# Optimization experiments

Measured on AMD Instinct MI355X. Metric: run time of the kernel, lower is better.

The kernel has to match this reference:

```python
import jax, jax.numpy as jnp
import numpy as np

# ---- module config (init kwargs) ----
EMB = 256
HIDDEN = 256
L, H, P = 4, 8, 4
CH = HIDDEN // H
PADDING_MODE = "zeros"   # 'zeros' or 'border'
ALIGN_CORNERS = False
# feature pyramid level shapes (height, width), static
SHAPES = np.array([[128, 128], [64, 64], [32, 32], [16, 16]], dtype=np.int32)
LEVEL_STARTS = np.concatenate([[0], np.cumsum(SHAPES.prod(-1))[:-1]]).astype(np.int32)

B, N = 8, 1024
I = int(SHAPES.prod(-1).sum())  # 21760


def setup_inputs() -> dict:
    key = jax.random.key(0)
    ks = jax.random.split(key, 8)
    scale = 0.02
    return {
        "img": jax.random.normal(ks[0], (B, I, EMB), jnp.float32),
        "img_shapes": jnp.asarray(SHAPES),
        "queries": jax.random.normal(ks[1], (B, N, EMB), jnp.float32),
        "reference_points": jax.random.uniform(ks[2], (B, N, 2), dtype=jnp.float32),
        "W_img": jax.random.normal(ks[3], (EMB, HIDDEN), jnp.float32) * scale,
        "b_img": jnp.zeros((HIDDEN,), jnp.float32),
        "W_q": jax.random.normal(ks[4], (EMB, H * L * P * 3), jnp.float32) * scale,
        "b_q": jnp.zeros((H * L * P * 3,), jnp.float32),
        "W_out": jax.random.normal(ks[5], (HIDDEN, EMB), jnp.float32) * scale,
        "b_out": jnp.zeros((EMB,), jnp.float32),
    }


def _msda(img, points, attn):
    """Multiscale deformable attention core.
    img:    [B, I, H, CH] flattened pyramid features
    points: [B, N, H, L, P, 2] (x, y) in [0, 1]
    attn:   [B, N, H, L, P]
    returns [B, N, H, CH]
    """
    b, _, h_, ch = img.shape
    n = points.shape[1]
    img_t = img.transpose(0, 2, 1, 3)  # [B, H, I, CH]
    levels = []
    for l in range(L):
        hh, ww = int(SHAPES[l, 0]), int(SHAPES[l, 1])
        start = int(LEVEL_STARTS[l])
        p = points[:, :, :, l]  # [B, N, H, P, 2]
        # grid_sample pixel mapping (after the module's 2*p-1 normalization)
        if ALIGN_CORNERS:
            x = p[..., 0] * (ww - 1)
            y = p[..., 1] * (hh - 1)
        else:
            x = p[..., 0] * ww - 0.5
            y = p[..., 1] * hh - 0.5
        x0 = jnp.floor(x); y0 = jnp.floor(y)
        wx = x - x0;       wy = y - y0
        x0i = x0.astype(jnp.int32); y0i = y0.astype(jnp.int32)
        acc = jnp.zeros((b, h_, n * P, ch), img.dtype)
        corners = [
            (x0i,     y0i,     (1 - wx) * (1 - wy)),
            (x0i + 1, y0i,     wx * (1 - wy)),
            (x0i,     y0i + 1, (1 - wx) * wy),
            (x0i + 1, y0i + 1, wx * wy),
        ]
        for xi, yi, cw in corners:
            if PADDING_MODE == "zeros":
                valid = (xi >= 0) & (xi < ww) & (yi >= 0) & (yi < hh)
                cw = cw * valid.astype(cw.dtype)
            xc = jnp.clip(xi, 0, ww - 1)
            yc = jnp.clip(yi, 0, hh - 1)
            idx = start + yc * ww + xc                              # [B, N, H, P]
            idx_t = idx.transpose(0, 2, 1, 3).reshape(b, h_, n * P)  # [B, H, N*P]
            g = jnp.take_along_axis(img_t, idx_t[..., None], axis=2)  # [B, H, N*P, CH]
            cw_t = cw.transpose(0, 2, 1, 3).reshape(b, h_, n * P, 1)
            acc = acc + cw_t * g
        levels.append(acc.reshape(b, h_, n, P, ch))
    samples = jnp.stack(levels, axis=3)            # [B, H, N, L, P, CH]
    attn_t = attn.transpose(0, 2, 1, 3, 4)          # [B, H, N, L, P]
    return jnp.einsum("bhnlpc,bhnlp->bnhc", samples, attn_t)


def reference(img, img_shapes, queries, reference_points, W_img, b_img, W_q, b_q, W_out, b_out):
    b, i_, _ = img.shape
    n = queries.shape[1]
    qp = (queries @ W_q + b_q).reshape(b, n, H, L, P, 3)
    offsets = qp[..., :2]                            # [B, N, H, L, P, 2]
    attn = jax.nn.softmax(qp[..., 2].reshape(b, n, H, L * P), axis=-1).reshape(b, n, H, L, P)
    img_p = (img @ W_img + b_img).reshape(b, i_, H, CH)
    shapes_f = img_shapes.astype(jnp.float32)        # [L, 2] (h, w)
    # faithful to source: offsets / img_shapes[:, None, :]
    sampling_points = reference_points[:, :, None, None, None, :] + offsets / shapes_f[:, None, :]
    out = _msda(img_p, sampling_points, attn)        # [B, N, H, CH]
    return out.reshape(b, n, HIDDEN) @ W_out + b_out
```

## Files before the change

### kernel.cpp

```cpp
#include <hip/hip_runtime.h>
#include <type_traits>
#include <utility>

#define B_    8
#define NQ_   1024
#define I_    21760
#define EMB_  256
#define HID_  256
#define H_    8
#define CH_   32

typedef float  f32x4  __attribute__((ext_vector_type(4)));
typedef __bf16 bf16x8 __attribute__((ext_vector_type(8)));
typedef short  s16x8  __attribute__((ext_vector_type(8)));

template <typename V, typename = void>
struct bf16_mfma_native : std::false_type {};
template <typename V>
struct bf16_mfma_native<V, std::void_t<decltype(__builtin_amdgcn_mfma_f32_16x16x32_bf16(
    std::declval<V>(), std::declval<V>(), std::declval<f32x4>(), 0, 0, 0))>>
    : std::true_type {};

template <typename V>
__device__ __forceinline__ f32x4 mfma_dispatch(V a, V b, f32x4 c) {
  if constexpr (bf16_mfma_native<V>::value) {
    return __builtin_amdgcn_mfma_f32_16x16x32_bf16(a, b, c, 0, 0, 0);
  } else {
    return __builtin_amdgcn_mfma_f32_16x16x32_bf16(
        __builtin_bit_cast(s16x8, a), __builtin_bit_cast(s16x8, b), c, 0, 0, 0);
  }
}

__device__ __forceinline__ f32x4 MFMA(s16x8 a, s16x8 b, f32x4 c) {
  return mfma_dispatch(__builtin_bit_cast(bf16x8, a), __builtin_bit_cast(bf16x8, b), c);
}

__device__ __forceinline__ unsigned short f2bf(float f) {
  unsigned u = __float_as_uint(f);
  u += 0x7fffu + ((u >> 16) & 1u);
  return (unsigned short)(u >> 16);
}

__global__ __launch_bounds__(512) void convert_w(
    const float* __restrict__ Wi, const float* __restrict__ Wq,
    const float* __restrict__ Wo, unsigned* __restrict__ wib,
    unsigned* __restrict__ wqb, unsigned* __restrict__ wob) {
  const int g = blockIdx.x * 512 + threadIdx.x;
  const float* S;
  unsigned* D;
  int N, t;
  if (g < 32768)      { S = Wi; D = wib; N = 256; t = g; }
  else if (g < 81920) { S = Wq; D = wqb; N = 384; t = g - 32768; }
  else                { S = Wo; D = wob; N = 256; t = g - 81920; }
  const int col = t >> 7, k = (t & 127) << 1;
  const unsigned lo = f2bf(S[(size_t)k * N + col]);
  const unsigned hi = f2bf(S[(size_t)(k + 1) * N + col]);
  D[t] = lo | (hi << 16);
}

template <int NS, int OUTM>
__device__ __forceinline__ void gemm_phase(
    const float* __restrict__ A, const unsigned short* __restrict__ Wb,
    const float* __restrict__ bias, void* __restrict__ Out,
    const int N, const int Mtiles, short* __restrict__ lds,
    const int bid0, const int nblk) {
  const int tid  = threadIdx.x;
  const int lane = tid & 63;
  const int wave = tid >> 6;
  const int quad = lane >> 4;
  const int ln   = lane & 15;

  float bv[NS];
#pragma unroll
  for (int st = 0; st < NS; ++st) bv[st] = bias[st * 128 + wave * 16 + ln];

  const unsigned short* wbase = Wb + (size_t)(wave * 16 + ln) * 256 + quad * 8;

  const int sr = tid >> 4;
  const int sc = (tid & 15) * 16;

  int t = bid0;
  if (t >= Mtiles) { return; }

  float4 v0, v1, v2, v3;
  {
    const float4* src = (const float4*)(A + ((size_t)t * 32 + sr) * 256 + sc);
    v0 = src[0]; v1 = src[1]; v2 = src[2]; v3 = src[3];
    s16x8 p0, p1;
    p0[0] = (short)f2bf(v0.x); p0[1] = (short)f2bf(v0.y);
    p0[2] = (short)f2bf(v0.z); p0[3] = (short)f2bf(v0.w);
    p0[4] = (short)f2bf(v1.x); p0[5] = (short)f2bf(v1.y);
    p0[6] = (short)f2bf(v1.z); p0[7] = (short)f2bf(v1.w);
    p1[0] = (short)f2bf(v2.x); p1[1] = (short)f2bf(v2.y);
    p1[2] = (short)f2bf(v2.z); p1[3] = (short)f2bf(v2.w);
    p1[4] = (short)f2bf(v3.x); p1[5] = (short)f2bf(v3.y);
    p1[6] = (short)f2bf(v3.z); p1[7] = (short)f2bf(v3.w);
    *(s16x8*)&lds[sr * 264 + sc]     = p0;
    *(s16x8*)&lds[sr * 264 + sc + 8] = p1;
  }
  __syncthreads();

  int cur = 0;
  for (; t < Mtiles; t += nblk) {
    const int tn = t + nblk;
    if (tn < Mtiles) {
      const float4* src = (const float4*)(A + ((size_t)tn * 32 + sr) * 256 + sc);
      v0 = src[0]; v1 = src[1]; v2 = src[2]; v3 = src[3];
    }

    short* buf = lds + cur * (32 * 264);
    f32x4 acc[NS][2];
#pragma unroll
    for (int st = 0; st < NS; ++st) {
      acc[st][0] = f32x4{bv[st], bv[st], bv[st], bv[st]};
      acc[st][1] = acc[st][0];
    }
#pragma unroll
    for (int ks = 0; ks < 8; ++ks) {
      s16x8 a0 = *(const s16x8*)&buf[ln * 264 + ks * 32 + quad * 8];
      s16x8 a1 = *(const s16x8*)&buf[(ln + 16) * 264 + ks * 32 + quad * 8];
#pragma unroll
      for (int st = 0; st < NS; ++st) {
        const s16x8 wf = *(const s16x8*)&wbase[(size_t)st * 128 * 256 + ks * 32];
        acc[st][0] = MFMA(a0, wf, acc[st][0]);
        acc[st][1] = MFMA(a1, wf, acc[st][1]);
      }
    }

    const size_t rowBase = (size_t)t * 32;
    if constexpr (OUTM == 1) {
      const int tb  = (int)(rowBase / I_);
      const int ir0 = (int)(rowBase - (size_t)tb * I_);
      unsigned short* O = (unsigned short*)Out;
#pragma unroll
      for (int st = 0; st < NS; ++st) {
        const int ng = st * 128 + wave * 16 + ln;
        const int hh = ng >> 5, cc = ng & 31;
        const size_t pl = (size_t)(tb * 8 + hh) * I_;
#pragma unroll
        for (int rt = 0; rt < 2; ++rt) {
#pragma unroll
          for (int r = 0; r < 4; ++r) {
            const size_t i = pl + (size_t)(ir0 + rt * 16 + quad * 4 + r);
            O[i * 32 + cc] = f2bf(acc[st][rt][r]);
          }
        }
      }
    } else {
      float* O = (float*)Out;
#pragma unroll
      for (int st = 0; st < NS; ++st) {
        const int ng = st * 128 + wave * 16 + ln;
#pragma unroll
        for (int rt = 0; rt < 2; ++rt) {
#pragma unroll
          for (int r = 0; r < 4; ++r) {
            const size_t m = rowBase + rt * 16 + quad * 4 + r;
            O[m * N + ng] = acc[st][rt][r];
          }
        }
      }
    }

    if (tn < Mtiles) {
      short* nbuf = lds + (cur ^ 1) * (32 * 264);
      s16x8 p0, p1;
      p0[0] = (short)f2bf(v0.x); p0[1] = (short)f2bf(v0.y);
      p0[2] = (short)f2bf(v0.z); p0[3] = (short)f2bf(v0.w);
      p0[4] = (short)f2bf(v1.x); p0[5] = (short)f2bf(v1.y);
      p0[6] = (short)f2bf(v1.z); p0[7] = (short)f2bf(v1.w);
      p1[0] = (short)f2bf(v2.x); p1[1] = (short)f2bf(v2.y);
      p1[2] = (short)f2bf(v2.z); p1[3] = (short)f2bf(v2.w);
      p1[4] = (short)f2bf(v3.x); p1[5] = (short)f2bf(v3.y);
      p1[6] = (short)f2bf(v3.z); p1[7] = (short)f2bf(v3.w);
      *(s16x8*)&nbuf[sr * 264 + sc]     = p0;
      *(s16x8*)&nbuf[sr * 264 + sc + 8] = p1;
    }
    __syncthreads();
    cur ^= 1;
  }
}

__global__ __launch_bounds__(512) void proj_kernel(
    const float* __restrict__ img, const float* __restrict__ queries,
    const unsigned short* __restrict__ wib, const float* __restrict__ b_img,
    const unsigned short* __restrict__ wqb, const float* __restrict__ b_q,
    unsigned short* __restrict__ imgp, float* __restrict__ qp) {
  __shared__ __align__(16) short lds[2 * 32 * 264];
  if (blockIdx.x < 704) {
    gemm_phase<2, 1>(img, wib, b_img, (void*)imgp, 256, (B_ * I_) / 32,
                     lds, blockIdx.x, 704);
  } else {
    gemm_phase<3, 0>(queries, wqb, b_q, (void*)qp, 384, (B_ * NQ_) / 32,
                     lds, (int)blockIdx.x - 704, 64);
  }
}

__global__ __launch_bounds__(256) void msda_out_kernel(
    const unsigned int* __restrict__ imgp,
    const float* __restrict__ qp, const float* __restrict__ refp,
    const unsigned short* __restrict__ wob, const float* __restrict__ b_out,
    float* __restrict__ out) {
  __shared__ __align__(16) float sw[1024][4];
  __shared__ __align__(16) int   sib[1024][2];
  __shared__ __align__(16) short lA[16 * 264];
  const int blk = blockIdx.x;
  const int b   = blk & 7;
  const int n0  = (blk >> 3) << 4;
  const int tid = threadIdx.x;

  for (int half = 0; half < 2; ++half) {
#pragma unroll
    for (int it = 0; it < 4; ++it) {
      const int item = it * 256 + tid;
      const int lp = item & 15, gh = item >> 4;
      const int q8 = gh >> 3, h = gh & 7;
      const int l = lp >> 2;
      const int ww = 128 >> l;
      const int start = (65536 - (65536 >> (2 * l))) / 3;
      const float invsh = __uint_as_float((unsigned)(120 + l) << 23);

      const int n   = n0 + (half << 3) + q8;
      const int bid = (b << 10) | n;
      const float* qb = qp + (size_t)bid * 384 + h * 48 + lp * 3;
      const float ox = qb[0], oy = qb[1], z = qb[2];
      float m = z;
      m = fmaxf(m, __shfl_xor(m, 1, 16));
      m = fmaxf(m, __shfl_xor(m, 2, 16));
      m = fmaxf(m, __shfl_xor(m, 4, 16));
      m = fmaxf(m, __shfl_xor(m, 8, 16));
      float e = __expf(z - m);
      float s = e;
      s += __shfl_xor(s, 1, 16);
      s += __shfl_xor(s, 2, 16);
      s += __shfl_xor(s, 4, 16);
      s += __shfl_xor(s, 8, 16);
      const float a = e / s;

      const float rx = refp[bid * 2], ry = refp[bid * 2 + 1];
      const float px = (rx + ox * invsh) * (float)ww - 0.5f;
      const float py = (ry + oy * invsh) * (float)ww - 0.5f;
      const float x0f = floorf(px), y0f = floorf(py);
      const float wx = px - x0f, wy = py - y0f;
      const int x0 = (int)x0f, y0 = (int)y0f;

      const int xb = min(max(x0, 0), ww - 2);
      float u0 = 0.f, u1 = 0.f;
      if (x0 >= 0 && x0 < ww)         { if (x0 == xb)     u0 += 1.f - wx; else u1 += 1.f - wx; }
      if (x0 + 1 >= 0 && x0 + 1 < ww) { if (x0 + 1 == xb) u0 += wx;       else u1 += wx; }
      const float wy0 = (y0 >= 0     && y0 < ww)     ? a * (1.f - wy) : 0.f;
      const float wy1 = (y0 + 1 >= 0 && y0 + 1 < ww) ? a * wy         : 0.f;
      const int yc0 = min(max(y0, 0), ww - 1);
      const int yc1 = min(max(y0 + 1, 0), ww - 1);

      const int pb = (b * 8 + h) * I_ + start + xb;
      sw[item][0] = wy0 * u0; sw[item][1] = wy0 * u1;
      sw[item][2] = wy1 * u0; sw[item][3] = wy1 * u1;
      sib[item][0] = (pb + yc0 * ww) * 16;
      sib[item][1] = (pb + yc1 * ww) * 16;
    }
    __syncthreads();

#pragma unroll
    for (int it = 0; it < 4; ++it) {
      const int item = it * 256 + tid;
      const int c2 = item & 15, gh = item >> 4;
      const int q8 = gh >> 3, h = gh & 7;
      const int p  = c2 >> 3;
      const int cp = ((c2 & 7) << 1) + (p << 4);
      float a0 = 0.f, a1 = 0.f, a2 = 0.f, a3 = 0.f;
#pragma unroll
      for (int lp = 0; lp < 16; ++lp) {
        const float4 w4 = *(const float4*)sw[gh * 16 + lp];
        const int2   ib = *(const int2*)sib[gh * 16 + lp];
        const float w0 = p ? w4.y : w4.x;
        const float w1 = p ? w4.w : w4.z;
        const uint2 ua = *(const uint2*)&imgp[ib.x + cp];
        const uint2 ub = *(const uint2*)&imgp[ib.y + cp];
        a0 += w0 * __uint_as_float(ua.x << 16);
        a1 += w0 * __uint_as_float(ua.x & 0xffff0000u);
        a2 += w0 * __uint_as_float(ua.y << 16);
        a3 += w0 * __uint_as_float(ua.y & 0xffff0000u);
        a0 += w1 * __uint_as_float(ub.x << 16);
        a1 += w1 * __uint_as_float(ub.x & 0xffff0000u);
        a2 += w1 * __uint_as_float(ub.y << 16);
        a3 += w1 * __uint_as_float(ub.y & 0xffff0000u);
      }
      a0 += __shfl_xor(a0, 8);
      a1 += __shfl_xor(a1, 8);
      a2 += __shfl_xor(a2, 8);
      a3 += __shfl_xor(a3, 8);
      const float rx = p ? a2 : a0;
      const float ry = p ? a3 : a1;
      const int row = (half << 3) + q8;
      const unsigned pr = (unsigned)f2bf(rx) | ((unsigned)f2bf(ry) << 16);
      *(unsigned*)&lA[row * 264 + h * 32 + ((c2 & 7) << 2) + (p << 1)] = pr;
    }
    __syncthreads();
  }

  const int lane = tid & 63, wv = tid >> 6;
  const int quad = lane >> 4, ln = lane & 15;
  f32x4 acc[4];
#pragma unroll
  for (int s = 0; s < 4; ++s) {
    const float bb = b_out[wv * 64 + s * 16 + ln];
    acc[s] = f32x4{bb, bb, bb, bb};
  }
#pragma unroll
  for (int ks = 0; ks < 8; ++ks) {
    const s16x8 a = *(const s16x8*)&lA[ln * 264 + ks * 32 + quad * 8];
#pragma unroll
    for (int s = 0; s < 4; ++s) {
      const int ng = wv * 64 + s * 16 + ln;
      const s16x8 wf = *(const s16x8*)&wob[(size_t)ng * 256 + ks * 32 + quad * 8];
      acc[s] = MFMA(a, wf, acc[s]);
    }
  }
#pragma unroll
  for (int s = 0; s < 4; ++s) {
    const int ng = wv * 64 + s * 16 + ln;
#pragma unroll
    for (int r = 0; r < 4; ++r) {
      const int m = quad * 4 + r;
      out[(size_t)(b * 1024 + n0 + m) * 256 + ng] = acc[s][r];
    }
  }
}

#define OFF_IMGP 0ULL
#define OFF_QP   89128960ULL
#define OFF_WIB  101711872ULL
#define OFF_WQB  101842944ULL
#define OFF_WOB  102039552ULL
#define WS_NEEDED 102170624ULL

extern "C" void kernel_launch(void* const* d_in, const int* in_sizes, int n_in,
                              void* d_out, int out_size, void* d_ws, size_t ws_size,
                              hipStream_t stream) {
  const float* img     = (const float*)d_in[0];
  const float* queries = (const float*)d_in[2];
  const float* refp    = (const float*)d_in[3];
  const float* W_img   = (const float*)d_in[4];
  const float* b_img   = (const float*)d_in[5];
  const float* W_q     = (const float*)d_in[6];
  const float* b_q     = (const float*)d_in[7];
  const float* W_out   = (const float*)d_in[8];
  const float* b_out   = (const float*)d_in[9];

  if (ws_size < WS_NEEDED) return;

  char* ws = (char*)d_ws;
  unsigned short* imgp = (unsigned short*)(ws + OFF_IMGP);
  float* qp            = (float*)(ws + OFF_QP);
  unsigned short* wib  = (unsigned short*)(ws + OFF_WIB);
  unsigned short* wqb  = (unsigned short*)(ws + OFF_WQB);
  unsigned short* wob  = (unsigned short*)(ws + OFF_WOB);

  hipLaunchKernelGGL(convert_w, dim3(224), dim3(512), 0, stream,
                     W_img, W_q, W_out,
                     (unsigned*)wib, (unsigned*)wqb, (unsigned*)wob);
  hipLaunchKernelGGL(proj_kernel, dim3(768), dim3(512), 0, stream,
                     img, queries, wib, b_img, wqb, b_q, imgp, qp);
  hipLaunchKernelGGL(msda_out_kernel, dim3(512), dim3(256), 0, stream,
                     (const unsigned int*)imgp, qp, refp, wob, b_out,
                     (float*)d_out);
}
```

Baseline: 323.4 us.

## Use 64-row GEMM tiles with single LDS buffer in projection kernel

The projection GEMM now processes 64 rows per tile instead of 32, so each weight fragment loaded from global memory feeds four MFMAs instead of two. The LDS double buffer becomes a single 64-row buffer: the next tile's global loads are issued into registers before the MFMAs, and conversion and storing happen at the top of the next iteration. The grid shrinks from 768 to 512 blocks and launch bounds request 4 blocks per CU. The trade-off is more registers per thread and an extra barrier per tile, which could limit occupancy or latency hiding.

New measurement: 372.2 us. 15.1% more time.

```diff
diff --git a/kernel.cpp b/kernel.cpp
--- a/kernel.cpp
+++ b/kernel.cpp
@@ -39,6 +39,11 @@
   unsigned u = __float_as_uint(f);
   u += 0x7fffu + ((u >> 16) & 1u);
   return (unsigned short)(u >> 16);
+}
+
+__device__ __forceinline__ void pack4(s16x8& p, int o, float4 v) {
+  p[o + 0] = (short)f2bf(v.x); p[o + 1] = (short)f2bf(v.y);
+  p[o + 2] = (short)f2bf(v.z); p[o + 3] = (short)f2bf(v.w);
 }
 
 __global__ __launch_bounds__(512) void convert_w(
@@ -76,58 +81,63 @@
 
   const unsigned short* wbase = Wb + (size_t)(wave * 16 + ln) * 256 + quad * 8;
 
-  const int sr = tid >> 4;
-  const int sc = (tid & 15) * 16;
+  const int sr = tid >> 3;
+  const int sc = (tid & 7) * 32;
 
   int t = bid0;
   if (t >= Mtiles) { return; }
 
-  float4 v0, v1, v2, v3;
+  float4 v0, v1, v2, v3, v4, v5, v6, v7;
   {
-    const float4* src = (const float4*)(A + ((size_t)t * 32 + sr) * 256 + sc);
+    const float4* src = (const float4*)(A + ((size_t)t * 64 + sr) * 256 + sc);
     v0 = src[0]; v1 = src[1]; v2 = src[2]; v3 = src[3];
-    s16x8 p0, p1;
-    p0[0] = (short)f2bf(v0.x); p0[1] = (short)f2bf(v0.y);
-    p0[2] = (short)f2bf(v0.z); p0[3] = (short)f2bf(v0.w);
-    p0[4] = (short)f2bf(v1.x); p0[5] = (short)f2bf(v1.y);
-    p0[6] = (short)f2bf(v1.z); p0[7] = (short)f2bf(v1.w);
-    p1[0] = (short)f2bf(v2.x); p1[1] = (short)f2bf(v2.y);
-    p1[2] = (short)f2bf(v2.z); p1[3] = (short)f2bf(v2.w);
-    p1[4] = (short)f2bf(v3.x); p1[5] = (short)f2bf(v3.y);
-    p1[6] = (short)f2bf(v3.z); p1[7] = (short)f2bf(v3.w);
-    *(s16x8*)&lds[sr * 264 + sc]     = p0;
-    *(s16x8*)&lds[sr * 264 + sc + 8] = p1;
-  }
-  __syncthreads();
-
-  int cur = 0;
+    v4 = src[4]; v5 = src[5]; v6 = src[6]; v7 = src[7];
+  }
+
   for (; t < Mtiles; t += nblk) {
+    {
+      s16x8 p0, p1, p2, p3;
+      pack4(p0, 0, v0); pack4(p0, 4, v1);
+      pack4(p1, 0, v2); pack4(p1, 4, v3);
+      pack4(p2, 0, v4); pack4(p2, 4, v5);
+      pack4(p3, 0, v6); pack4(p3, 4, v7);
+      *(s16x8*)&lds[sr * 264 + sc]      = p0;
+      *(s16x8*)&lds[sr * 264 + sc + 8]  = p1;
+      *(s16x8*)&lds[sr * 264 + sc + 16] = p2;
+      *(s16x8*)&lds[sr * 264 + sc + 24] = p3;
+    }
+    __syncthreads();
+
     const int tn = t + nblk;
     if (tn < Mtiles) {
-      const float4* src = (const float4*)(A + ((size_t)tn * 32 + sr) * 256 + sc);
+      const float4* src = (const float4*)(A + ((size_t)tn * 64 + sr) * 256 + sc);
       v0 = src[0]; v1 = src[1]; v2 = src[2]; v3 = src[3];
-    }
-
-    short* buf = lds + cur * (32 * 264);
-    f32x4 acc[NS][2];
-#pragma unroll
-    for (int st = 0; st < NS; ++st) {
-      acc[st][0] = f32x4{bv[st], bv[st], bv[st], bv[st]};
-      acc[st][1] = acc[st][0];
-    }
+      v4 = src[4]; v5 = src[5]; v6 = src[6]; v7 = src[7];
+    }
+
+    f32x4 acc[NS][4];
+#pragma unroll
+    for (int st = 0; st < NS; ++st)
+#pragma unroll
+      for (int rt = 0; rt < 4; ++rt)
+        acc[st][rt] = f32x4{bv[st], bv[st], bv[st], bv[st]};
 #pragma unroll
     for (int ks = 0; ks < 8; ++ks) {
-      s16x8 a0 = *(const s16x8*)&buf[ln * 264 + ks * 32 + quad * 8];
-      s16x8 a1 = *(const s16x8*)&buf[(ln + 16) * 264 + ks * 32 + quad * 8];
+      s16x8 a0 = *(const s16x8*)&lds[ln * 264 + ks * 32 + quad * 8];
+      s16x8 a1 = *(const s16x8*)&lds[(ln + 16) * 264 + ks * 32 + quad * 8];
+      s16x8 a2 = *(const s16x8*)&lds[(ln + 32) * 264 + ks * 32 + quad * 8];
+      s16x8 a3 = *(const s16x8*)&lds[(ln + 48) * 264 + ks * 32 + quad * 8];
 #pragma unroll
       for (int st = 0; st < NS; ++st) {
         const s16x8 wf = *(const s16x8*)&wbase[(size_t)st * 128 * 256 + ks * 32];
         acc[st][0] = MFMA(a0, wf, acc[st][0]);
         acc[st][1] = MFMA(a1, wf, acc[st][1]);
+        acc[st][2] = MFMA(a2, wf, acc[st][2]);
+        acc[st][3] = MFMA(a3, wf, acc[st][3]);
       }
     }
 
-    const size_t rowBase = (size_t)t * 32;
+    const size_t rowBase = (size_t)t * 64;
     if constexpr (OUTM == 1) {
       const int tb  = (int)(rowBase / I_);
       const int ir0 = (int)(rowBase - (size_t)tb * I_);
@@ -138,7 +148,7 @@
         const int hh = ng >> 5, cc = ng & 31;
         const size_t pl = (size_t)(tb * 8 + hh) * I_;
 #pragma unroll
-        for (int rt = 0; rt < 2; ++rt) {
+        for (int rt = 0; rt < 4; ++rt) {
 #pragma unroll
           for (int r = 0; r < 4; ++r) {
             const size_t i = pl + (size_t)(ir0 + rt * 16 + quad * 4 + r);
@@ -152,7 +162,7 @@
       for (int st = 0; st < NS; ++st) {
         const int ng = st * 128 + wave * 16 + ln;
 #pragma unroll
-        for (int rt = 0; rt < 2; ++rt) {
+        for (int rt = 0; rt < 4; ++rt) {
 #pragma unroll
           for (int r = 0; r < 4; ++r) {
             const size_t m = rowBase + rt * 16 + quad * 4 + r;
@@ -161,38 +171,22 @@
         }
       }
     }
-
-    if (tn < Mtiles) {
-      short* nbuf = lds + (cur ^ 1) * (32 * 264);
-      s16x8 p0, p1;
-      p0[0] = (short)f2bf(v0.x); p0[1] = (short)f2bf(v0.y);
-      p0[2] = (short)f2bf(v0.z); p0[3] = (short)f2bf(v0.w);
-      p0[4] = (short)f2bf(v1.x); p0[5] = (short)f2bf(v1.y);
-      p0[6] = (short)f2bf(v1.z); p0[7] = (short)f2bf(v1.w);
-      p1[0] = (short)f2bf(v2.x); p1[1] = (short)f2bf(v2.y);
-      p1[2] = (short)f2bf(v2.z); p1[3] = (short)f2bf(v2.w);
-      p1[4] = (short)f2bf(v3.x); p1[5] = (short)f2bf(v3.y);
-      p1[6] = (short)f2bf(v3.z); p1[7] = (short)f2bf(v3.w);
-      *(s16x8*)&nbuf[sr * 264 + sc]     = p0;
-      *(s16x8*)&nbuf[sr * 264 + sc + 8] = p1;
-    }
     __syncthreads();
-    cur ^= 1;
-  }
-}
-
-__global__ __launch_bounds__(512) void proj_kernel(
+  }
+}
+
+__global__ __launch_bounds__(512, 4) void proj_kernel(
     const float* __restrict__ img, const float* __restrict__ queries,
     const unsigned short* __restrict__ wib, const float* __restrict__ b_img,
     const unsigned short* __restrict__ wqb, const float* __restrict__ b_q,
     unsigned short* __restrict__ imgp, float* __restrict__ qp) {
-  __shared__ __align__(16) short lds[2 * 32 * 264];
-  if (blockIdx.x < 704) {
-    gemm_phase<2, 1>(img, wib, b_img, (void*)imgp, 256, (B_ * I_) / 32,
-                     lds, blockIdx.x, 704);
+  __shared__ __align__(16) short lds[64 * 264];
+  if (blockIdx.x < 448) {
+    gemm_phase<2, 1>(img, wib, b_img, (void*)imgp, 256, (B_ * I_) / 64,
+                     lds, blockIdx.x, 448);
   } else {
-    gemm_phase<3, 0>(queries, wqb, b_q, (void*)qp, 384, (B_ * NQ_) / 32,
-                     lds, (int)blockIdx.x - 704, 64);
+    gemm_phase<3, 0>(queries, wqb, b_q, (void*)qp, 384, (B_ * NQ_) / 64,
+                     lds, (int)blockIdx.x - 448, 64);
   }
 }
 
@@ -360,7 +354,7 @@
   hipLaunchKernelGGL(convert_w, dim3(224), dim3(512), 0, stream,
                      W_img, W_q, W_out,
                      (unsigned*)wib, (unsigned*)wqb, (unsigned*)wob);
-  hipLaunchKernelGGL(proj_kernel, dim3(768), dim3(512), 0, stream,
+  hipLaunchKernelGGL(proj_kernel, dim3(512), dim3(512), 0, stream,
                      img, queries, wib, b_img, wqb, b_q, imgp, qp);
   hipLaunchKernelGGL(msda_out_kernel, dim3(512), dim3(256), 0, stream,
                      (const unsigned int*)imgp, qp, refp, wob, b_out,
```
